# Performance work log

Hardware: AMD Instinct MI355X
Metric: run time of the kernel (lower is better)

## Reference

```python
import jax, jax.numpy as jnp
import numpy as np

TOP_K = 20  # MemoryBank top_k default in eval path (softmax_w_top)


def setup_inputs() -> dict:
    key = jax.random.key(0)
    k1, k2, k3, k4 = jax.random.split(key, 4)
    B, CK, CV = 2, 64, 256
    NM, NQ = 32768, 4096  # memory entries (8 frames x 64x64), query entries (64x64)
    return {
        "mk": jax.random.normal(k1, (B, CK, NM), dtype=jnp.float32),
        "qk": jax.random.normal(k2, (B, CK, NQ), dtype=jnp.float32),
        "mv0": jax.random.normal(k3, (B, CV, NM), dtype=jnp.float32),
        "mv1": jax.random.normal(k4, (B, CV, NM), dtype=jnp.float32),
    }


def reference(mk, qk, mv0, mv1):
    # mk: [B, CK, NM], qk: [B, CK, NQ], mv*: [B, CV, NM]
    B, CK, NM = mk.shape
    NQ = qk.shape[-1]
    # affinity = (-||mk||^2 + 2*mk^T qk) / sqrt(CK)   (negative-L2 + dot score)
    a = jnp.sum(mk * mk, axis=1)                        # [B, NM]
    b = 2.0 * jnp.einsum('bcm,bcq->bmq', mk, qk)        # [B, NM, NQ]
    aff = (b - a[:, :, None]) / jnp.sqrt(jnp.asarray(CK, mk.dtype))
    # top-k softmax over the memory dim, scattered back to a sparse dense matrix
    aff_t = jnp.swapaxes(aff, 1, 2)                     # [B, NQ, NM]
    vals, idx = jax.lax.top_k(aff_t, TOP_K)             # [B, NQ, K]
    w = jax.nn.softmax(vals, axis=-1)
    bi = jnp.arange(B)[:, None, None]
    qi = jnp.arange(NQ)[None, :, None]
    sparse = jnp.zeros_like(aff_t).at[bi, qi, idx].set(w)
    affinity = jnp.swapaxes(sparse, 1, 2)               # [B, NM, NQ]
    # per-value bmm readout sharing one affinity
    r0 = jnp.einsum('bcm,bmq->bcq', mv0, affinity)      # [B, CV, NQ]
    r1 = jnp.einsum('bcm,bmq->bcq', mv1, affinity)
    return (r0, r1)
```

## Files before the change

kernel.cpp:

```cpp
#include <hip/hip_runtime.h>
#include <hip/hip_bf16.h>
#include <cstdint>

#define B_  2
#define CK_ 64
#define NM_ 32768
#define NQ_ 4096
#define CV_ 256
#define K_  20

typedef unsigned short ushort_t;
typedef unsigned int uint_t;
typedef unsigned long long u64_t;
typedef float f32x4 __attribute__((ext_vector_type(4)));
typedef float f32x16 __attribute__((ext_vector_type(16)));
typedef short short8v __attribute__((ext_vector_type(8)));

__device__ __forceinline__ ushort_t f2bf_rn(float f) {
  uint_t x = __float_as_uint(f);
  uint_t r = x + 0x7FFFu + ((x >> 16) & 1u);
  return (ushort_t)(r >> 16);
}
__device__ __forceinline__ float bf2f(ushort_t u) {
  return __uint_as_float(((uint_t)u) << 16);
}

__global__ __launch_bounds__(256) void prep_mk(const float* __restrict__ mk,
                                               ushort_t* __restrict__ mkt,
                                               ushort_t* __restrict__ mlt,
                                               float* __restrict__ ans) {
  int i = blockIdx.x * 256 + threadIdx.x;
  int b = i >> 15, m = i & (NM_ - 1);
  const float* src = mk + (size_t)b * CK_ * NM_ + m;
  const size_t chbase = ((size_t)(b * 1024 + (m >> 5)) << 11);
  const int ml = m & 31;
  float s = 0.f;
  #pragma unroll
  for (int c8 = 0; c8 < 8; ++c8) {
    ushort_t hh[8], ll[8];
    #pragma unroll
    for (int j = 0; j < 8; ++j) {
      float v = src[(size_t)(c8 * 8 + j) * NM_];
      s = fmaf(v, v, s);
      ushort_t h = f2bf_rn(v);
      hh[j] = h;
      ll[j] = f2bf_rn(v - bf2f(h));
    }
    size_t off = chbase + (c8 << 8) + (ml << 3);
    *reinterpret_cast<short8v*>(mkt + off) = *reinterpret_cast<short8v*>(hh);
    *reinterpret_cast<short8v*>(mlt + off) = *reinterpret_cast<short8v*>(ll);
  }
  ans[i] = -0.125f * s;
}

__global__ __launch_bounds__(256) void prep_qk(const float* __restrict__ qk,
                                               ushort_t* __restrict__ qkh,
                                               ushort_t* __restrict__ qkl) {
  int i = blockIdx.x * 256 + threadIdx.x;
  int b = i >> 12, q = i & (NQ_ - 1);
  const float* src = qk + (size_t)b * CK_ * NQ_ + q;
  ushort_t* dh = qkh + (size_t)i * CK_;
  ushort_t* dl = qkl + (size_t)i * CK_;
  #pragma unroll
  for (int c8 = 0; c8 < 8; ++c8) {
    ushort_t hh[8], ll[8];
    #pragma unroll
    for (int j = 0; j < 8; ++j) {
      float v = 0.25f * src[(size_t)(c8 * 8 + j) * NQ_];
      ushort_t h = f2bf_rn(v);
      hh[j] = h;
      ll[j] = f2bf_rn(v - bf2f(h));
    }
    *reinterpret_cast<short8v*>(dh + c8 * 8) = *reinterpret_cast<short8v*>(hh);
    *reinterpret_cast<short8v*>(dl + c8 * 8) = *reinterpret_cast<short8v*>(ll);
  }
}

__global__ __launch_bounds__(256) void transpose_mv(const float* __restrict__ mv0,
                                                    const float* __restrict__ mv1,
                                                    ushort_t* __restrict__ mvt0,
                                                    ushort_t* __restrict__ mvt1) {
  __shared__ float tl[64][33];
  const int zz = blockIdx.z;
  const int bank = zz & 1, b = zz >> 1;
  const float* src = (bank ? mv1 : mv0) + (size_t)b * CV_ * NM_;
  ushort_t*    dst = (bank ? mvt1 : mvt0) + (size_t)b * NM_ * CV_;
  const int m0 = blockIdx.x * 32, c0 = blockIdx.y * 64;
  const int t = threadIdx.x;
  #pragma unroll
  for (int i = 0; i < 8; ++i) {
    int f = t + 256 * i;
    int c = f >> 5, ml = f & 31;
    tl[c][ml] = src[(size_t)(c0 + c) * NM_ + m0 + ml];
  }
  __syncthreads();
  int m = t >> 3, c8 = t & 7;
  ushort_t pack[8];
  #pragma unroll
  for (int j = 0; j < 8; ++j) pack[j] = f2bf_rn(tl[c8 * 8 + j][m]);
  *reinterpret_cast<short8v*>(dst + (size_t)(m0 + m) * CV_ + c0 + c8 * 8) =
      *reinterpret_cast<short8v*>(pack);
}

#define TKF_FOR(F) F(0) F(1) F(2) F(3) F(4) F(5) F(6) F(7) F(8) F(9) F(10) F(11) F(12) F(13) F(14) F(15) F(16) F(17) F(18) F(19)
#define TKF_DECL(J) float tv##J = -3.4e38f; int ti##J = 0;

#define TKF_SW(A,B) { bool c_ = tv##B > tv##A; \
  float fx_ = fmaxf(tv##A, tv##B); float fn_ = fminf(tv##A, tv##B); \
  int ix_ = c_ ? ti##B : ti##A;    int in_ = c_ ? ti##A : ti##B; \
  tv##A = fx_; tv##B = fn_; ti##A = ix_; ti##B = in_; }

#define TKF_INS(S,M) { if ((S) > tv19) { tv19 = (S); ti19 = (M); \
  TKF_SW(18,19) TKF_SW(17,18) TKF_SW(16,17) TKF_SW(15,16) TKF_SW(14,15) \
  TKF_SW(13,14) TKF_SW(12,13) TKF_SW(11,12) TKF_SW(10,11) TKF_SW(9,10) \
  TKF_SW(8,9) TKF_SW(7,8) TKF_SW(6,7) TKF_SW(5,6) TKF_SW(4,5) \
  TKF_SW(3,4) TKF_SW(2,3) TKF_SW(1,2) TKF_SW(0,1) } }

#define TKF_PUSH(S,M) { float s_ = (S); if (s_ > thr) { \
  fifoW[cnt << 6] = (((u64_t)(uint_t)__float_as_uint(s_)) << 32) | (uint_t)(M); ++cnt; } }

#define TKF_DRAIN_FIFO() { \
  _Pragma("clang loop unroll(disable)") \
  for (int d_ = 0; d_ < 16; ++d_) { \
    if (__all(cnt <= d_)) break; \
    u64_t pk_ = fifoW[d_ << 6]; \
    float s_ = __uint_as_float((uint_t)(pk_ >> 32)); \
    int m_ = (int)(uint_t)pk_; \
    if (d_ < cnt) { TKF_INS(s_, m_) } \
  } \
  cnt = 0; thr = tv19; }

#define TKF_CHK() { if (__any(cnt >= 8)) { TKF_DRAIN_FIFO() } }

#define MFMA32(A,B,C) __builtin_amdgcn_mfma_f32_32x32x16_bf16((A),(B),(C),0,0,0)

#define GLOAD_LDS16(G, L) __builtin_amdgcn_global_load_lds( \
    (__attribute__((address_space(1))) unsigned int*)(G), \
    (__attribute__((address_space(3))) unsigned int*)(L), 16, 0, 0)

__global__ __launch_bounds__(256, 2) void score_topk_mfma(
    const ushort_t* __restrict__ mkt, const ushort_t* __restrict__ mlt,
    const ushort_t* __restrict__ qkh, const ushort_t* __restrict__ qkl,
    const float* __restrict__ ans,
    float* __restrict__ pvals, int* __restrict__ pidx) {
  __shared__ __attribute__((aligned(16))) ushort_t ldsH[2 * 2048];
  __shared__ __attribute__((aligned(16))) ushort_t ldsL[2 * 2048];
  __shared__ __attribute__((aligned(16))) float    ldsA[2 * 32];
  __shared__ __attribute__((aligned(16))) u64_t    fifo[4][16][64];
  const int t = threadIdx.x;
  const int b = blockIdx.z, seg = blockIdx.y, qblk = blockIdx.x;
  const int segcnt = gridDim.y;
  const int chunks = (NM_ / 32) / segcnt;
  const int w = t >> 6, l = t & 63;
  const int lq = l & 31, hi = l >> 5;
  const int q = qblk * 128 + w * 32 + lq;
  const int gch0 = seg * chunks;

  u64_t* fifoW = &fifo[w][0][l];

  const size_t qbase = (((size_t)b * NQ_ + q) << 6) + hi * 8;
  const short8v bh0 = *(const short8v*)(qkh + qbase);
  const short8v bh1 = *(const short8v*)(qkh + qbase + 16);
  const short8v bh2 = *(const short8v*)(qkh + qbase + 32);
  const short8v bh3 = *(const short8v*)(qkh + qbase + 48);
  const short8v bl0 = *(const short8v*)(qkl + qbase);
  const short8v bl1 = *(const short8v*)(qkl + qbase + 16);
  const short8v bl2 = *(const short8v*)(qkl + qbase + 32);
  const short8v bl3 = *(const short8v*)(qkl + qbase + 48);

  TKF_FOR(TKF_DECL)
  float thr = -3.4e38f;
  int cnt = 0;

#define STAGE(NBUF, GCH) { \
  const size_t cb_ = ((size_t)(b * 1024) + (GCH)) << 11; \
  GLOAD_LDS16(mkt + cb_ + (((w << 6) + l) << 3), &ldsH[(NBUF) * 2048 + (w << 9)]); \
  GLOAD_LDS16(mlt + cb_ + (((w << 6) + l) << 3), &ldsL[(NBUF) * 2048 + (w << 9)]); \
  if (t < 8) GLOAD_LDS16(ans + ((size_t)b << 15) + ((GCH) << 5) + (t << 2), &ldsA[(NBUF) * 32]); \
}

#define COMPUTE(CH, BUF) \
  int chn_ = (CH) + 1; if (chn_ > chunks - 1) chn_ = chunks - 1; \
  STAGE(1 - (BUF), gch0 + chn_) \
  const int fro_ = (BUF) * 2048 + (hi << 8) + (lq << 3); \
  const short8v ah0 = *(const short8v*)&ldsH[fro_ + 0 * 512]; \
  const short8v ah1 = *(const short8v*)&ldsH[fro_ + 1 * 512]; \
  const short8v ah2 = *(const short8v*)&ldsH[fro_ + 2 * 512]; \
  const short8v ah3 = *(const short8v*)&ldsH[fro_ + 3 * 512]; \
  const short8v al0 = *(const short8v*)&ldsL[fro_ + 0 * 512]; \
  const short8v al1 = *(const short8v*)&ldsL[fro_ + 1 * 512]; \
  const short8v al2 = *(const short8v*)&ldsL[fro_ + 2 * 512]; \
  const short8v al3 = *(const short8v*)&ldsL[fro_ + 3 * 512]; \
  const float* ap_ = &ldsA[(BUF) * 32 + (hi << 2)]; \
  f32x4 an_a = *(const f32x4*)ap_; \
  f32x4 an_b = *(const f32x4*)(ap_ + 8); \
  f32x4 an_c = *(const f32x4*)(ap_ + 16); \
  f32x4 an_d = *(const f32x4*)(ap_ + 24); \
  f32x16 acc; \
  acc[0]  = an_a[0]; acc[1]  = an_a[1]; acc[2]  = an_a[2]; acc[3]  = an_a[3]; \
  acc[4]  = an_b[0]; acc[5]  = an_b[1]; acc[6]  = an_b[2]; acc[7]  = an_b[3]; \
  acc[8]  = an_c[0]; acc[9]  = an_c[1]; acc[10] = an_c[2]; acc[11] = an_c[3]; \
  acc[12] = an_d[0]; acc[13] = an_d[1]; acc[14] = an_d[2]; acc[15] = an_d[3]; \
  acc = MFMA32(ah0, bh0, acc); \
  acc = MFMA32(ah1, bh1, acc); \
  acc = MFMA32(ah2, bh2, acc); \
  acc = MFMA32(ah3, bh3, acc); \
  acc = MFMA32(ah0, bl0, acc); \
  acc = MFMA32(ah1, bl1, acc); \
  acc = MFMA32(ah2, bl2, acc); \
  acc = MFMA32(ah3, bl3, acc); \
  acc = MFMA32(al0, bh0, acc); \
  acc = MFMA32(al1, bh1, acc); \
  acc = MFMA32(al2, bh2, acc); \
  acc = MFMA32(al3, bh3, acc); \
  const int mb = ((gch0 + (CH)) << 5) + (hi << 2);

#define ITER(CH, BUF) { \
  COMPUTE(CH, BUF) \
  TKF_PUSH(acc[0], mb + 0)  TKF_PUSH(acc[1], mb + 1)  TKF_PUSH(acc[2], mb + 2)  TKF_PUSH(acc[3], mb + 3)  \
  TKF_PUSH(acc[4], mb + 8)  TKF_PUSH(acc[5], mb + 9)  TKF_PUSH(acc[6], mb + 10) TKF_PUSH(acc[7], mb + 11) \
  TKF_CHK() \
  TKF_PUSH(acc[8], mb + 16) TKF_PUSH(acc[9], mb + 17) TKF_PUSH(acc[10],mb + 18) TKF_PUSH(acc[11],mb + 19) \
  TKF_PUSH(acc[12],mb + 24) TKF_PUSH(acc[13],mb + 25) TKF_PUSH(acc[14],mb + 26) TKF_PUSH(acc[15],mb + 27) \
  TKF_CHK() \
  __syncthreads(); \
}

#define ITER_WARM(CH, BUF) { \
  COMPUTE(CH, BUF) \
  TKF_INS(acc[0], mb + 0)  TKF_INS(acc[1], mb + 1)  TKF_INS(acc[2], mb + 2)  TKF_INS(acc[3], mb + 3)  \
  TKF_INS(acc[4], mb + 8)  TKF_INS(acc[5], mb + 9)  TKF_INS(acc[6], mb + 10) TKF_INS(acc[7], mb + 11) \
  TKF_INS(acc[8], mb + 16) TKF_INS(acc[9], mb + 17) TKF_INS(acc[10],mb + 18) TKF_INS(acc[11],mb + 19) \
  TKF_INS(acc[12],mb + 24) TKF_INS(acc[13],mb + 25) TKF_INS(acc[14],mb + 26) TKF_INS(acc[15],mb + 27) \
  thr = tv19; \
  __syncthreads(); \
}

  STAGE(0, gch0)
  __syncthreads();

  ITER_WARM(0, 0)
  ITER(1, 1)
  #pragma clang loop unroll(disable)
  for (int ch2 = 1; ch2 < chunks / 2; ++ch2) {
    const int ch = ch2 * 2;
    ITER(ch, 0)
    ITER(ch + 1, 1)
  }
  if (__any(cnt > 0)) { TKF_DRAIN_FIFO() }

#undef ITER
#undef ITER_WARM
#undef COMPUTE
#undef STAGE

  const int part = (seg << 1) + hi;
  const int parts = segcnt << 1;
  float* pv = pvals + (((size_t)((b * parts + part) * K_)) << 12) + q;
  int*   pi = pidx  + (((size_t)((b * parts + part) * K_)) << 12) + q;
#define TKF_STORE(J) { pv[(size_t)(J) << 12] = tv##J; pi[(size_t)(J) << 12] = ti##J; }
  TKF_FOR(TKF_STORE)
#undef TKF_STORE
}

__global__ __launch_bounds__(256) void merge_kernel(const float* __restrict__ pvals,
                                                    const int* __restrict__ pidx,
                                                    float* __restrict__ fw,
                                                    int* __restrict__ fidx, int S) {
  int i = blockIdx.x * 256 + threadIdx.x;
  int b = i >> 12, q = i & (NQ_ - 1);

  float vals[K_]; int idxs[K_];
  #pragma unroll
  for (int j = 0; j < K_; ++j) { vals[j] = -3.4e38f; idxs[j] = 0; }

  for (int seg = 0; seg < S; ++seg) {
    const float* pp = pvals + (((size_t)((b * S + seg) * K_)) << 12) + q;
    const int*   qq = pidx  + (((size_t)((b * S + seg) * K_)) << 12) + q;
    #pragma clang loop unroll(disable)
    for (int j = 0; j < K_; ++j) {
      float v = pp[(size_t)j << 12];
      if (__all(v <= vals[K_ - 1])) break;
      if (v > vals[K_ - 1]) {
        int m = qq[(size_t)j << 12];
        vals[K_ - 1] = v; idxs[K_ - 1] = m;
        #pragma unroll
        for (int jj = K_ - 1; jj > 0; --jj) {
          if (vals[jj] > vals[jj - 1]) {
            float tv = vals[jj]; vals[jj] = vals[jj - 1]; vals[jj - 1] = tv;
            int   ti = idxs[jj]; idxs[jj] = idxs[jj - 1]; idxs[jj - 1] = ti;
          }
        }
      }
    }
  }

  float mx = vals[0];
  float w[K_]; float sum = 0.f;
  #pragma unroll
  for (int j = 0; j < K_; ++j) { w[j] = expf(vals[j] - mx); sum += w[j]; }
  float inv = 1.f / sum;
  #pragma unroll
  for (int j = 0; j < K_; ++j) {
    size_t o = (size_t)(b * K_ + j) * NQ_ + q;
    fw[o] = w[j] * inv; fidx[o] = idxs[j];
  }
}

__global__ __launch_bounds__(256) void readout_bf16(const ushort_t* __restrict__ mvt0,
                                                    const ushort_t* __restrict__ mvt1,
                                                    const float* __restrict__ fw,
                                                    const int* __restrict__ fidx,
                                                    float* __restrict__ out) {
  __shared__ float mw[16][K_];
  __shared__ int   mi[16][K_];
  __shared__ float ob0[256][17];
  __shared__ float ob1[256][17];
  const int t = threadIdx.x;
  const int b = blockIdx.y;
  const int q0 = blockIdx.x * 16;

  for (int i = t; i < 16 * K_; i += 256) {
    int qp = i / K_, k = i % K_;
    size_t o = (size_t)(b * K_ + k) * NQ_ + q0 + qp;
    mw[qp][k] = fw[o];
    mi[qp][k] = fidx[o];
  }
  __syncthreads();

  const int c2 = (t & 127) * 2, hq = t >> 7;
  for (int qp = hq * 8; qp < hq * 8 + 8; ++qp) {
    float a00 = 0.f, a01 = 0.f, a10 = 0.f, a11 = 0.f;
    #pragma unroll 5
    for (int k = 0; k < K_; ++k) {
      int m = mi[qp][k]; float ww = mw[qp][k];
      size_t o = ((size_t)(b * NM_ + m) << 8) + c2;
      uint_t v0 = *reinterpret_cast<const uint_t*>(mvt0 + o);
      uint_t v1 = *reinterpret_cast<const uint_t*>(mvt1 + o);
      a00 = fmaf(ww, __uint_as_float(v0 << 16), a00);
      a01 = fmaf(ww, __uint_as_float(v0 & 0xFFFF0000u), a01);
      a10 = fmaf(ww, __uint_as_float(v1 << 16), a10);
      a11 = fmaf(ww, __uint_as_float(v1 & 0xFFFF0000u), a11);
    }
    ob0[c2][qp] = a00; ob0[c2 + 1][qp] = a01;
    ob1[c2][qp] = a10; ob1[c2 + 1][qp] = a11;
  }
  __syncthreads();

  float* out0 = out + (size_t)b * CV_ * NQ_;
  float* out1 = out + (size_t)B_ * CV_ * NQ_ + (size_t)b * CV_ * NQ_;
  for (int i = t; i < 256 * 16; i += 256) {
    int c = i >> 4, qp = i & 15;
    out0[(size_t)c * NQ_ + q0 + qp] = ob0[c][qp];
    out1[(size_t)c * NQ_ + q0 + qp] = ob1[c][qp];
  }
}

__global__ __launch_bounds__(256) void readout_f32(const float* __restrict__ v0src,
                                                   const float* __restrict__ v1src,
                                                   const float* __restrict__ fw,
                                                   const int* __restrict__ fidx,
                                                   float* __restrict__ out) {
  __shared__ float mw[16][K_];
  __shared__ int   mi[16][K_];
  __shared__ float ob0[256][17];
  __shared__ float ob1[256][17];
  const int t = threadIdx.x;
  const int b = blockIdx.y;
  const int q0 = blockIdx.x * 16;

  for (int i = t; i < 16 * K_; i += 256) {
    int qp = i / K_, k = i % K_;
    size_t o = (size_t)(b * K_ + k) * NQ_ + q0 + qp;
    mw[qp][k] = fw[o];
    mi[qp][k] = fidx[o];
  }
  __syncthreads();

  for (int qp = 0; qp < 16; ++qp) {
    float a0 = 0.f, a1 = 0.f;
    #pragma unroll 5
    for (int k = 0; k < K_; ++k) {
      int m = mi[qp][k]; float ww = mw[qp][k];
      size_t o = (size_t)b * CV_ * NM_ + (size_t)t * NM_ + m;
      a0 = fmaf(ww, v0src[o], a0);
      a1 = fmaf(ww, v1src[o], a1);
    }
    ob0[t][qp] = a0; ob1[t][qp] = a1;
  }
  __syncthreads();

  float* out0 = out + (size_t)b * CV_ * NQ_;
  float* out1 = out + (size_t)B_ * CV_ * NQ_ + (size_t)b * CV_ * NQ_;
  for (int i = t; i < 256 * 16; i += 256) {
    int c = i >> 4, qp = i & 15;
    out0[(size_t)c * NQ_ + q0 + qp] = ob0[c][qp];
    out1[(size_t)c * NQ_ + q0 + qp] = ob1[c][qp];
  }
}

extern "C" void kernel_launch(void* const* d_in, const int* in_sizes, int n_in,
                              void* d_out, int out_size, void* d_ws, size_t ws_size,
                              hipStream_t stream) {
  (void)in_sizes; (void)n_in; (void)out_size;
  const float* mk  = (const float*)d_in[0];
  const float* qk  = (const float*)d_in[1];
  const float* mv0 = (const float*)d_in[2];
  const float* mv1 = (const float*)d_in[3];
  float* out = (float*)d_out;

  auto al = [](size_t x) { return (x + 255) & ~(size_t)255; };
  const size_t mkB  = (size_t)B_ * NM_ * CK_ * 2;
  const size_t qkB  = (size_t)B_ * NQ_ * CK_ * 2;
  const size_t anB  = (size_t)B_ * NM_ * 4;
  const size_t finB = (size_t)B_ * K_ * NQ_ * 4;
  const size_t tpB  = (size_t)B_ * NM_ * CV_ * 2;
  auto prtB = [](int parts) { return (size_t)B_ * parts * K_ * NQ_ * 4; };
  auto core = [&](int parts) {
    return 2 * al(mkB) + 2 * al(qkB) + al(anB) + 2 * al(prtB(parts)) + 2 * al(finB);
  };

  int segcnt; bool tp;
  if      (ws_size >= core(16) + 2 * al(tpB)) { segcnt = 8; tp = true;  }
  else if (ws_size >= core(16))               { segcnt = 8; tp = false; }
  else                                        { segcnt = 4; tp = false; }
  const int parts = segcnt * 2;

  char* p = (char*)d_ws;
  ushort_t* mkt = (ushort_t*)p; p += al(mkB);
  ushort_t* mlt = (ushort_t*)p; p += al(mkB);
  ushort_t* qkh = (ushort_t*)p; p += al(qkB);
  ushort_t* qkl = (ushort_t*)p; p += al(qkB);
  float* ans    = (float*)p;    p += al(anB);
  float* pvals  = (float*)p;    p += al(prtB(parts));
  int*   pidx   = (int*)p;      p += al(prtB(parts));
  float* fw     = (float*)p;    p += al(finB);
  int*   fidx   = (int*)p;      p += al(finB);
  ushort_t* mvt0 = nullptr, * mvt1 = nullptr;
  if (tp) { mvt0 = (ushort_t*)p; p += al(tpB); mvt1 = (ushort_t*)p; p += al(tpB); }

  prep_mk<<<B_ * NM_ / 256, 256, 0, stream>>>(mk, mkt, mlt, ans);
  prep_qk<<<B_ * NQ_ / 256, 256, 0, stream>>>(qk, qkh, qkl);
  if (tp)
    transpose_mv<<<dim3(NM_ / 32, CV_ / 64, B_ * 2), 256, 0, stream>>>(mv0, mv1, mvt0, mvt1);
  score_topk_mfma<<<dim3(NQ_ / 128, segcnt, B_), 256, 0, stream>>>(mkt, mlt, qkh, qkl, ans, pvals, pidx);
  merge_kernel<<<B_ * NQ_ / 256, 256, 0, stream>>>(pvals, pidx, fw, fidx, parts);
  if (tp) readout_bf16<<<dim3(NQ_ / 16, B_), 256, 0, stream>>>(mvt0, mvt1, fw, fidx, out);
  else    readout_f32<<<dim3(NQ_ / 16, B_), 256, 0, stream>>>(mv0, mv1, fw, fidx, out);
}
```

Before: 548.9 us.

## Software-pipeline MFMA scoring with top-k scan of previous chunk, share threshold

Restructures the score/top-k loop so the MFMAs for chunk N are issued while the top-k FIFO push scan runs on chunk N-1's accumulator, using two ping-pong accumulators and a tail scan. The 12-MFMA dependent chain is split into two independent accumulator chains that are summed at the end, which shortens the serial latency. The pruning threshold is also shared between the two half-waves that serve the same query via a lane shuffle, so fewer candidates get pushed. The costs are more live registers (two 16-float accumulators), which may hurt at the 2-waves launch bound, and a slightly different fp32 summation order.

```diff
diff --git a/kernel.cpp b/kernel.cpp
--- a/kernel.cpp
+++ b/kernel.cpp
@@ -8,6 +8,7 @@
 #define NQ_ 4096
 #define CV_ 256
 #define K_  20
+#define FDEPTH_ 16
 
 typedef unsigned short ushort_t;
 typedef unsigned int uint_t;
@@ -121,14 +122,15 @@
 
 #define TKF_DRAIN_FIFO() { \
   _Pragma("clang loop unroll(disable)") \
-  for (int d_ = 0; d_ < 16; ++d_) { \
+  for (int d_ = 0; d_ < FDEPTH_; ++d_) { \
     if (__all(cnt <= d_)) break; \
     u64_t pk_ = fifoW[d_ << 6]; \
     float s_ = __uint_as_float((uint_t)(pk_ >> 32)); \
     int m_ = (int)(uint_t)pk_; \
     if (d_ < cnt) { TKF_INS(s_, m_) } \
   } \
-  cnt = 0; thr = tv19; }
+  cnt = 0; thr = tv19; \
+  thr = fmaxf(thr, __shfl_xor(thr, 32)); }
 
 #define TKF_CHK() { if (__any(cnt >= 8)) { TKF_DRAIN_FIFO() } }
 
@@ -146,7 +148,7 @@
   __shared__ __attribute__((aligned(16))) ushort_t ldsH[2 * 2048];
   __shared__ __attribute__((aligned(16))) ushort_t ldsL[2 * 2048];
   __shared__ __attribute__((aligned(16))) float    ldsA[2 * 32];
-  __shared__ __attribute__((aligned(16))) u64_t    fifo[4][16][64];
+  __shared__ __attribute__((aligned(16))) u64_t    fifo[4][FDEPTH_][64];
   const int t = threadIdx.x;
   const int b = blockIdx.z, seg = blockIdx.y, qblk = blockIdx.x;
   const int segcnt = gridDim.y;
@@ -179,9 +181,9 @@
   if (t < 8) GLOAD_LDS16(ans + ((size_t)b << 15) + ((GCH) << 5) + (t << 2), &ldsA[(NBUF) * 32]); \
 }
 
-#define COMPUTE(CH, BUF) \
-  int chn_ = (CH) + 1; if (chn_ > chunks - 1) chn_ = chunks - 1; \
-  STAGE(1 - (BUF), gch0 + chn_) \
+#define ITER_P(CH, BUF, ACC, SCANSTMT) { \
+  { int chn_ = (CH) + 1; if (chn_ > chunks - 1) chn_ = chunks - 1; \
+    STAGE(1 - (BUF), gch0 + chn_) } \
   const int fro_ = (BUF) * 2048 + (hi << 8) + (lq << 3); \
   const short8v ah0 = *(const short8v*)&ldsH[fro_ + 0 * 512]; \
   const short8v ah1 = *(const short8v*)&ldsH[fro_ + 1 * 512]; \
@@ -196,62 +198,62 @@
   f32x4 an_b = *(const f32x4*)(ap_ + 8); \
   f32x4 an_c = *(const f32x4*)(ap_ + 16); \
   f32x4 an_d = *(const f32x4*)(ap_ + 24); \
-  f32x16 acc; \
-  acc[0]  = an_a[0]; acc[1]  = an_a[1]; acc[2]  = an_a[2]; acc[3]  = an_a[3]; \
-  acc[4]  = an_b[0]; acc[5]  = an_b[1]; acc[6]  = an_b[2]; acc[7]  = an_b[3]; \
-  acc[8]  = an_c[0]; acc[9]  = an_c[1]; acc[10] = an_c[2]; acc[11] = an_c[3]; \
-  acc[12] = an_d[0]; acc[13] = an_d[1]; acc[14] = an_d[2]; acc[15] = an_d[3]; \
-  acc = MFMA32(ah0, bh0, acc); \
-  acc = MFMA32(ah1, bh1, acc); \
-  acc = MFMA32(ah2, bh2, acc); \
-  acc = MFMA32(ah3, bh3, acc); \
-  acc = MFMA32(ah0, bl0, acc); \
-  acc = MFMA32(ah1, bl1, acc); \
-  acc = MFMA32(ah2, bl2, acc); \
-  acc = MFMA32(ah3, bl3, acc); \
-  acc = MFMA32(al0, bh0, acc); \
-  acc = MFMA32(al1, bh1, acc); \
-  acc = MFMA32(al2, bh2, acc); \
-  acc = MFMA32(al3, bh3, acc); \
-  const int mb = ((gch0 + (CH)) << 5) + (hi << 2);
-
-#define ITER(CH, BUF) { \
-  COMPUTE(CH, BUF) \
-  TKF_PUSH(acc[0], mb + 0)  TKF_PUSH(acc[1], mb + 1)  TKF_PUSH(acc[2], mb + 2)  TKF_PUSH(acc[3], mb + 3)  \
-  TKF_PUSH(acc[4], mb + 8)  TKF_PUSH(acc[5], mb + 9)  TKF_PUSH(acc[6], mb + 10) TKF_PUSH(acc[7], mb + 11) \
+  f32x16 c1_, c2_; \
+  c1_[0]  = an_a[0]; c1_[1]  = an_a[1]; c1_[2]  = an_a[2]; c1_[3]  = an_a[3]; \
+  c1_[4]  = an_b[0]; c1_[5]  = an_b[1]; c1_[6]  = an_b[2]; c1_[7]  = an_b[3]; \
+  c1_[8]  = an_c[0]; c1_[9]  = an_c[1]; c1_[10] = an_c[2]; c1_[11] = an_c[3]; \
+  c1_[12] = an_d[0]; c1_[13] = an_d[1]; c1_[14] = an_d[2]; c1_[15] = an_d[3]; \
+  c2_ = 0.f; \
+  c1_ = MFMA32(ah0, bh0, c1_);  c2_ = MFMA32(ah0, bl0, c2_); \
+  c1_ = MFMA32(ah1, bh1, c1_);  c2_ = MFMA32(al0, bh0, c2_); \
+  c1_ = MFMA32(ah2, bh2, c1_);  c2_ = MFMA32(ah1, bl1, c2_); \
+  c1_ = MFMA32(ah3, bh3, c1_);  c2_ = MFMA32(al1, bh1, c2_); \
+  c2_ = MFMA32(ah2, bl2, c2_); \
+  c2_ = MFMA32(al2, bh2, c2_); \
+  c2_ = MFMA32(ah3, bl3, c2_); \
+  c2_ = MFMA32(al3, bh3, c2_); \
+  SCANSTMT \
+  ACC = c1_ + c2_; \
+  __syncthreads(); \
+}
+
+#define SCANP(ACC, CHP) { \
+  const int mbp_ = ((gch0 + (CHP)) << 5) + (hi << 2); \
+  TKF_PUSH(ACC[0], mbp_ + 0)  TKF_PUSH(ACC[1], mbp_ + 1)  TKF_PUSH(ACC[2], mbp_ + 2)  TKF_PUSH(ACC[3], mbp_ + 3)  \
+  TKF_PUSH(ACC[4], mbp_ + 8)  TKF_PUSH(ACC[5], mbp_ + 9)  TKF_PUSH(ACC[6], mbp_ + 10) TKF_PUSH(ACC[7], mbp_ + 11) \
   TKF_CHK() \
-  TKF_PUSH(acc[8], mb + 16) TKF_PUSH(acc[9], mb + 17) TKF_PUSH(acc[10],mb + 18) TKF_PUSH(acc[11],mb + 19) \
-  TKF_PUSH(acc[12],mb + 24) TKF_PUSH(acc[13],mb + 25) TKF_PUSH(acc[14],mb + 26) TKF_PUSH(acc[15],mb + 27) \
-  TKF_CHK() \
-  __syncthreads(); \
-}
-
-#define ITER_WARM(CH, BUF) { \
-  COMPUTE(CH, BUF) \
-  TKF_INS(acc[0], mb + 0)  TKF_INS(acc[1], mb + 1)  TKF_INS(acc[2], mb + 2)  TKF_INS(acc[3], mb + 3)  \
-  TKF_INS(acc[4], mb + 8)  TKF_INS(acc[5], mb + 9)  TKF_INS(acc[6], mb + 10) TKF_INS(acc[7], mb + 11) \
-  TKF_INS(acc[8], mb + 16) TKF_INS(acc[9], mb + 17) TKF_INS(acc[10],mb + 18) TKF_INS(acc[11],mb + 19) \
-  TKF_INS(acc[12],mb + 24) TKF_INS(acc[13],mb + 25) TKF_INS(acc[14],mb + 26) TKF_INS(acc[15],mb + 27) \
+  TKF_PUSH(ACC[8], mbp_ + 16) TKF_PUSH(ACC[9], mbp_ + 17) TKF_PUSH(ACC[10], mbp_ + 18) TKF_PUSH(ACC[11], mbp_ + 19) \
+  TKF_PUSH(ACC[12], mbp_ + 24) TKF_PUSH(ACC[13], mbp_ + 25) TKF_PUSH(ACC[14], mbp_ + 26) TKF_PUSH(ACC[15], mbp_ + 27) \
+  TKF_CHK() }
+
+#define SCANW(ACC, CHP) { \
+  const int mbp_ = ((gch0 + (CHP)) << 5) + (hi << 2); \
+  TKF_INS(ACC[0], mbp_ + 0)  TKF_INS(ACC[1], mbp_ + 1)  TKF_INS(ACC[2], mbp_ + 2)  TKF_INS(ACC[3], mbp_ + 3)  \
+  TKF_INS(ACC[4], mbp_ + 8)  TKF_INS(ACC[5], mbp_ + 9)  TKF_INS(ACC[6], mbp_ + 10) TKF_INS(ACC[7], mbp_ + 11) \
+  TKF_INS(ACC[8], mbp_ + 16) TKF_INS(ACC[9], mbp_ + 17) TKF_INS(ACC[10], mbp_ + 18) TKF_INS(ACC[11], mbp_ + 19) \
+  TKF_INS(ACC[12], mbp_ + 24) TKF_INS(ACC[13], mbp_ + 25) TKF_INS(ACC[14], mbp_ + 26) TKF_INS(ACC[15], mbp_ + 27) \
   thr = tv19; \
-  __syncthreads(); \
-}
+  thr = fmaxf(thr, __shfl_xor(thr, 32)); }
+
+  f32x16 accA, accB;
 
   STAGE(0, gch0)
   __syncthreads();
 
-  ITER_WARM(0, 0)
-  ITER(1, 1)
+  ITER_P(0, 0, accA, {})
+  ITER_P(1, 1, accB, SCANW(accA, 0))
   #pragma clang loop unroll(disable)
-  for (int ch2 = 1; ch2 < chunks / 2; ++ch2) {
+  for (int ch2 = 1; ch2 <= chunks / 2 - 1; ++ch2) {
     const int ch = ch2 * 2;
-    ITER(ch, 0)
-    ITER(ch + 1, 1)
-  }
+    ITER_P(ch,     0, accA, SCANP(accB, ch - 1))
+    ITER_P(ch + 1, 1, accB, SCANP(accA, ch))
+  }
+  SCANP(accB, chunks - 1)
   if (__any(cnt > 0)) { TKF_DRAIN_FIFO() }
 
-#undef ITER
-#undef ITER_WARM
-#undef COMPUTE
+#undef ITER_P
+#undef SCANP
+#undef SCANW
 #undef STAGE
 
   const int part = (seg << 1) + hi;
```

Result: faster. 536.4 us (-2.3%).
